# Optimization experiments

Hardware: AMD Instinct MI355X
Metric: run time of the kernel (lower is better)

## Reference

```python
import jax, jax.numpy as jnp
import numpy as np

EPS = 1e-12  # torch F.normalize clamp_min eps
NUM_HEADS = 4


def setup_inputs() -> dict:
    key = jax.random.key(0)
    ks = jax.random.split(key, 6)
    B, N, C = 8, 8192, 256
    x1 = jax.random.normal(ks[0], (B, N, C), dtype=jnp.float32)
    x2 = jax.random.normal(ks[1], (B, N, C), dtype=jnp.float32)
    s = 1.0 / np.sqrt(C)
    Wq = jax.random.normal(ks[2], (C, C), dtype=jnp.float32) * s
    Wk = jax.random.normal(ks[3], (C, C), dtype=jnp.float32) * s
    Wv = jax.random.normal(ks[4], (C, C), dtype=jnp.float32) * s
    Wo = jax.random.normal(ks[5], (C, C), dtype=jnp.float32) * s
    bo = jnp.zeros((C,), dtype=jnp.float32)
    temperature = jnp.ones((NUM_HEADS, 1, 1), dtype=jnp.float32)
    return {"x1": x1, "x2": x2, "Wq": Wq, "Wk": Wk, "Wv": Wv,
            "Wo": Wo, "bo": bo, "temperature": temperature}


def reference(x1, x2, Wq, Wk, Wv, Wo, bo, temperature):
    B, N, C = x1.shape
    H = NUM_HEADS
    d = C // H
    # Linear projections (torch Linear: y = x W^T), then [B,H,d,N] layout
    q = (x1 @ Wq.T).reshape(B, N, H, d).transpose(0, 2, 3, 1)  # [B,H,d,N]
    k = (x2 @ Wk.T).reshape(B, N, H, d).transpose(0, 2, 3, 1)  # [B,H,d,N]
    v = (x2 @ Wv.T).reshape(B, N, H, d).transpose(0, 2, 3, 1)  # [B,H,d,N]
    # L2-normalize along the token axis (dim=-1)
    qn = q / jnp.maximum(jnp.linalg.norm(q, axis=-1, keepdims=True), EPS)
    kn = k / jnp.maximum(jnp.linalg.norm(k, axis=-1, keepdims=True), EPS)
    # Channel-wise cross-covariance attention: [B,H,d,d]
    attn = jnp.einsum('bhdn,bhen->bhde', qn, kn) * temperature
    attn = jax.nn.softmax(attn, axis=-1)
    # (dropout is identity in eval mode)
    x_cross = jnp.einsum('bhde,bhen->bhdn', attn, v)  # [B,H,d,N]
    x_cross = x_cross.transpose(0, 3, 1, 2).reshape(B, N, C)  # [B,N,C]
    return x_cross @ Wo.T + bo
```

## Files before the change

kernel.cpp:

```cpp
#include <hip/hip_runtime.h>
#include <hip/hip_bf16.h>

#define BDIM 8
#define NTOK 8192
#define CDIM 256
#define HEADS 4
#define DHEAD 64
#define MROWS (BDIM * NTOK)

typedef unsigned short ushort_t;
typedef short bf16x8 __attribute__((ext_vector_type(8)));
typedef float f32x4 __attribute__((ext_vector_type(4)));
typedef unsigned short u16x8 __attribute__((ext_vector_type(8)));

#define GLOAD16(g, l) __builtin_amdgcn_global_load_lds( \
    (const __attribute__((address_space(1))) unsigned int*)(g), \
    (__attribute__((address_space(3))) unsigned int*)(l), 16, 0, 0)

__device__ inline ushort_t f2bf(float f) {
    __hip_bfloat16 h = __float2bfloat16(f);
    return *reinterpret_cast<ushort_t*>(&h);
}

__global__ __launch_bounds__(256) void zero_kernel(float* __restrict__ p, int n) {
    int i = blockIdx.x * 256 + threadIdx.x;
    if (i < n) p[i] = 0.0f;
}

__global__ __launch_bounds__(256) void cvt_bf16(
    const float* __restrict__ x1, const float* __restrict__ x2,
    const float* __restrict__ Wq, const float* __restrict__ Wk,
    const float* __restrict__ Wv,
    ushort_t* __restrict__ xb1, ushort_t* __restrict__ xb2,
    ushort_t* __restrict__ Wqb, ushort_t* __restrict__ Wkb,
    ushort_t* __restrict__ Wvb)
{
    const float* s; ushort_t* d; int n;
    switch (blockIdx.y) {
        case 0: s = x1; d = xb1; n = 16777216; break;
        case 1: s = x2; d = xb2; n = 16777216; break;
        case 2: s = Wq; d = Wqb; n = 65536; break;
        case 3: s = Wk; d = Wkb; n = 65536; break;
        default: s = Wv; d = Wvb; n = 65536; break;
    }
    int i = (blockIdx.x * 256 + threadIdx.x) * 8;
    if (i >= n) return;
    float4 a = *(const float4*)&s[i];
    float4 b = *(const float4*)&s[i + 4];
    u16x8 o;
    o[0] = f2bf(a.x); o[1] = f2bf(a.y); o[2] = f2bf(a.z); o[3] = f2bf(a.w);
    o[4] = f2bf(b.x); o[5] = f2bf(b.y); o[6] = f2bf(b.z); o[7] = f2bf(b.w);
    *(u16x8*)&d[i] = o;
}

__global__ __launch_bounds__(256) void proj_mfma(
    const ushort_t* __restrict__ xb1, const ushort_t* __restrict__ xb2,
    const ushort_t* __restrict__ Wqb, const ushort_t* __restrict__ Wkb,
    const ushort_t* __restrict__ Wvb,
    ushort_t* __restrict__ qp, ushort_t* __restrict__ kp, ushort_t* __restrict__ vp,
    float* __restrict__ ssq, float* __restrict__ ssk)
{
    const ushort_t* A; const ushort_t* W; ushort_t* outp; float* ss;
    if (blockIdx.z == 0)      { A = xb1; W = Wqb; outp = qp; ss = ssq; }
    else if (blockIdx.z == 1) { A = xb2; W = Wkb; outp = kp; ss = ssk; }
    else                      { A = xb2; W = Wvb; outp = vp; ss = nullptr; }

    __shared__ ushort_t Asl[8192];
    __shared__ ushort_t Bsl[8192];
    __shared__ float colss[128];

    const int t = threadIdx.x;
    const int lane = t & 63, w = t >> 6;
    const int l16 = lane & 15, quad = lane >> 4;
    const int m0 = blockIdx.x * 128;
    const int c0 = blockIdx.y * 128;
    const int wm = (w >> 1) * 64, wn = (w & 1) * 64;

    f32x4 acc[4][4] = {};

    for (int k0 = 0; k0 < CDIM; k0 += 64) {
        __syncthreads();
#pragma unroll
        for (int r = 0; r < 4; ++r) {
            int slot = r * 256 + t;
            int kg = slot >> 7, m = slot & 127;
            GLOAD16(A + (size_t)(m0 + m) * CDIM + k0 + kg * 8,
                    &Asl[(size_t)(r * 256 + w * 64) * 8]);
        }
#pragma unroll
        for (int r = 0; r < 4; ++r) {
            int slot = r * 256 + t;
            int kg = slot >> 7, c = slot & 127;
            GLOAD16(W + (size_t)(c0 + c) * CDIM + k0 + kg * 8,
                    &Bsl[(size_t)(r * 256 + w * 64) * 8]);
        }
        __syncthreads();
#pragma unroll
        for (int ks = 0; ks < 2; ++ks) {
            const int kg = ks * 4 + quad;
            bf16x8 aF[4], bF[4];
#pragma unroll
            for (int i = 0; i < 4; ++i)
                aF[i] = *(const bf16x8*)&Asl[(size_t)(kg * 128 + wm + i * 16 + l16) * 8];
#pragma unroll
            for (int j = 0; j < 4; ++j)
                bF[j] = *(const bf16x8*)&Bsl[(size_t)(kg * 128 + wn + j * 16 + l16) * 8];
#pragma unroll
            for (int i = 0; i < 4; ++i)
#pragma unroll
                for (int j = 0; j < 4; ++j)
                    acc[i][j] = __builtin_amdgcn_mfma_f32_16x16x32_bf16(aF[i], bF[j], acc[i][j], 0, 0, 0);
        }
    }

#pragma unroll
    for (int i = 0; i < 4; ++i) {
#pragma unroll
        for (int j = 0; j < 4; ++j) {
            int col = c0 + wn + j * 16 + l16;
#pragma unroll
            for (int reg = 0; reg < 4; ++reg) {
                int row = m0 + wm + i * 16 + quad * 4 + reg;
                outp[(size_t)row * CDIM + col] = f2bf(acc[i][j][reg]);
            }
        }
    }

    if (ss) {
        if (t < 128) colss[t] = 0.0f;
        __syncthreads();
#pragma unroll
        for (int j = 0; j < 4; ++j) {
            float s = 0.0f;
#pragma unroll
            for (int i = 0; i < 4; ++i)
#pragma unroll
                for (int reg = 0; reg < 4; ++reg)
                    s += acc[i][j][reg] * acc[i][j][reg];
            atomicAdd(&colss[wn + j * 16 + l16], s);
        }
        __syncthreads();
        if (t < 128) {
            int b = m0 >> 13;
            atomicAdd(&ss[b * CDIM + c0 + t], colss[t]);
        }
    }
}

__global__ __launch_bounds__(256) void gram_mfma(
    const ushort_t* __restrict__ qp, const ushort_t* __restrict__ kp,
    float* __restrict__ G)
{
    constexpr int NS = 144;
    __shared__ ushort_t qs[64 * NS];
    __shared__ ushort_t ks2[64 * NS];
    __shared__ float gsum[4096];

    const int t = threadIdx.x;
    const int lane = t & 63, w = t >> 6;
    const int l16 = lane & 15, quad = lane >> 4;
    const int slab = blockIdx.x, h = blockIdx.y, b = blockIdx.z;
    const size_t base = (size_t)b * NTOK * CDIM + h * DHEAD;

    for (int i = t; i < 4096; i += 256) gsum[i] = 0.0f;

    f32x4 acc[4][4] = {};

    for (int n0 = slab * 512; n0 < slab * 512 + 512; n0 += 128) {
        __syncthreads();
#pragma unroll
        for (int r = 0; r < 4; ++r) {
            int idx = r * 256 + t;
            int n = idx & 127, c8 = idx >> 7;
            size_t g = base + (size_t)(n0 + n) * CDIM + c8 * 8;
            ushort4 qa = *(const ushort4*)&qp[g];
            ushort4 qb = *(const ushort4*)&qp[g + 4];
            ushort4 ka = *(const ushort4*)&kp[g];
            ushort4 kb = *(const ushort4*)&kp[g + 4];
            int c = c8 * 8;
            qs[(c + 0) * NS + n] = qa.x; qs[(c + 1) * NS + n] = qa.y;
            qs[(c + 2) * NS + n] = qa.z; qs[(c + 3) * NS + n] = qa.w;
            qs[(c + 4) * NS + n] = qb.x; qs[(c + 5) * NS + n] = qb.y;
            qs[(c + 6) * NS + n] = qb.z; qs[(c + 7) * NS + n] = qb.w;
            ks2[(c + 0) * NS + n] = ka.x; ks2[(c + 1) * NS + n] = ka.y;
            ks2[(c + 2) * NS + n] = ka.z; ks2[(c + 3) * NS + n] = ka.w;
            ks2[(c + 4) * NS + n] = kb.x; ks2[(c + 5) * NS + n] = kb.y;
            ks2[(c + 6) * NS + n] = kb.z; ks2[(c + 7) * NS + n] = kb.w;
        }
        __syncthreads();
        bf16x8 aF[4], bF[4];
#pragma unroll
        for (int i = 0; i < 4; ++i)
            aF[i] = *(const bf16x8*)&qs[(i * 16 + l16) * NS + w * 32 + quad * 8];
#pragma unroll
        for (int j = 0; j < 4; ++j)
            bF[j] = *(const bf16x8*)&ks2[(j * 16 + l16) * NS + w * 32 + quad * 8];
#pragma unroll
        for (int i = 0; i < 4; ++i)
#pragma unroll
            for (int j = 0; j < 4; ++j)
                acc[i][j] = __builtin_amdgcn_mfma_f32_16x16x32_bf16(aF[i], bF[j], acc[i][j], 0, 0, 0);
    }

    __syncthreads();
#pragma unroll
    for (int i = 0; i < 4; ++i)
#pragma unroll
        for (int j = 0; j < 4; ++j)
#pragma unroll
            for (int reg = 0; reg < 4; ++reg)
                atomicAdd(&gsum[(i * 16 + quad * 4 + reg) * 64 + j * 16 + l16], acc[i][j][reg]);
    __syncthreads();

    float* Gp = G + (size_t)(b * HEADS + h) * 4096;
    for (int i = t; i < 4096; i += 256) atomicAdd(&Gp[i], gsum[i]);
}

__global__ __launch_bounds__(64) void attn_softmax(
    float* __restrict__ G, const float* __restrict__ ssq,
    const float* __restrict__ ssk, const float* __restrict__ temp)
{
    const int h = blockIdx.x, b = blockIdx.y;
    const int d = threadIdx.x;
    __shared__ float nk[64];

    float nq = fmaxf(sqrtf(ssq[b * CDIM + h * DHEAD + d]), 1e-12f);
    nk[d]    = fmaxf(sqrtf(ssk[b * CDIM + h * DHEAD + d]), 1e-12f);
    __syncthreads();

    float* row = G + (size_t)(b * HEADS + h) * DHEAD * DHEAD + d * DHEAD;
    const float tmp = temp[h];

    float vals[64];
    float mx = -1e30f;
#pragma unroll
    for (int e = 0; e < 64; ++e) {
        float v = row[e] / (nq * nk[e]) * tmp;
        vals[e] = v;
        mx = fmaxf(mx, v);
    }
    float s = 0.0f;
#pragma unroll
    for (int e = 0; e < 64; ++e) {
        float ev = __expf(vals[e] - mx);
        vals[e] = ev;
        s += ev;
    }
    float inv = 1.0f / s;
#pragma unroll
    for (int e = 0; e < 64; ++e) row[e] = vals[e] * inv;
}

__global__ __launch_bounds__(256) void weff_kernel(
    const float* __restrict__ Wo, const float* __restrict__ attn,
    ushort_t* __restrict__ Weffb)
{
    const int h = blockIdx.x, b = blockIdx.y;
    const int c = threadIdx.x;
    __shared__ float at[64][65];

    const float* Ab = attn + (size_t)(b * HEADS + h) * DHEAD * DHEAD;
    for (int idx = c; idx < DHEAD * DHEAD; idx += 256)
        at[idx >> 6][idx & 63] = Ab[idx];
    __syncthreads();

    float wo[64];
#pragma unroll
    for (int d2 = 0; d2 < 64; ++d2) wo[d2] = Wo[(size_t)c * CDIM + h * DHEAD + d2];

    ushort_t* Wb = Weffb + (size_t)b * CDIM * CDIM + (size_t)c * CDIM + h * DHEAD;
#pragma unroll 4
    for (int e = 0; e < 64; ++e) {
        float s = 0.0f;
#pragma unroll
        for (int d2 = 0; d2 < 64; ++d2) s += wo[d2] * at[d2][e];
        Wb[e] = f2bf(s);
    }
}

__global__ __launch_bounds__(256) void out_mfma(
    const ushort_t* __restrict__ vp, const ushort_t* __restrict__ Weffb,
    const float* __restrict__ bo, float* __restrict__ out)
{
    __shared__ ushort_t Asl[8192];
    __shared__ ushort_t Bsl[8192];

    const int t = threadIdx.x;
    const int lane = t & 63, w = t >> 6;
    const int l16 = lane & 15, quad = lane >> 4;
    const int m0 = blockIdx.x * 128;
    const int c0 = blockIdx.y * 128;
    const int wm = (w >> 1) * 64, wn = (w & 1) * 64;
    const ushort_t* Wb = Weffb + (size_t)(m0 >> 13) * CDIM * CDIM;

    f32x4 acc[4][4] = {};

    for (int k0 = 0; k0 < CDIM; k0 += 64) {
        __syncthreads();
#pragma unroll
        for (int r = 0; r < 4; ++r) {
            int slot = r * 256 + t;
            int kg = slot >> 7, m = slot & 127;
            GLOAD16(vp + (size_t)(m0 + m) * CDIM + k0 + kg * 8,
                    &Asl[(size_t)(r * 256 + w * 64) * 8]);
        }
#pragma unroll
        for (int r = 0; r < 4; ++r) {
            int slot = r * 256 + t;
            int kg = slot >> 7, c = slot & 127;
            GLOAD16(Wb + (size_t)(c0 + c) * CDIM + k0 + kg * 8,
                    &Bsl[(size_t)(r * 256 + w * 64) * 8]);
        }
        __syncthreads();
#pragma unroll
        for (int ks = 0; ks < 2; ++ks) {
            const int kg = ks * 4 + quad;
            bf16x8 aF[4], bF[4];
#pragma unroll
            for (int i = 0; i < 4; ++i)
                aF[i] = *(const bf16x8*)&Asl[(size_t)(kg * 128 + wm + i * 16 + l16) * 8];
#pragma unroll
            for (int j = 0; j < 4; ++j)
                bF[j] = *(const bf16x8*)&Bsl[(size_t)(kg * 128 + wn + j * 16 + l16) * 8];
#pragma unroll
            for (int i = 0; i < 4; ++i)
#pragma unroll
                for (int j = 0; j < 4; ++j)
                    acc[i][j] = __builtin_amdgcn_mfma_f32_16x16x32_bf16(aF[i], bF[j], acc[i][j], 0, 0, 0);
        }
    }

#pragma unroll
    for (int i = 0; i < 4; ++i) {
#pragma unroll
        for (int j = 0; j < 4; ++j) {
            int col = c0 + wn + j * 16 + l16;
            float bias = bo[col];
#pragma unroll
            for (int reg = 0; reg < 4; ++reg) {
                int row = m0 + wm + i * 16 + quad * 4 + reg;
                out[(size_t)row * CDIM + col] = acc[i][j][reg] + bias;
            }
        }
    }
}

extern "C" void kernel_launch(void* const* d_in, const int* in_sizes, int n_in,
                              void* d_out, int out_size, void* d_ws, size_t ws_size,
                              hipStream_t stream) {
    const float* x1   = (const float*)d_in[0];
    const float* x2   = (const float*)d_in[1];
    const float* Wq   = (const float*)d_in[2];
    const float* Wk   = (const float*)d_in[3];
    const float* Wv   = (const float*)d_in[4];
    const float* Wo   = (const float*)d_in[5];
    const float* bo   = (const float*)d_in[6];
    const float* temp = (const float*)d_in[7];
    float* out = (float*)d_out;

    char* ws = (char*)d_ws;
    const size_t SZP = (size_t)MROWS * CDIM * sizeof(ushort_t);
    ushort_t* qp   = (ushort_t*)(ws);
    ushort_t* kp   = (ushort_t*)(ws + SZP);
    ushort_t* vp   = (ushort_t*)(ws + 2 * SZP);
    ushort_t* xb1  = (ushort_t*)(ws + 3 * SZP);
    ushort_t* xb2  = (ushort_t*)(ws + 4 * SZP);
    ushort_t* Wqb  = (ushort_t*)(ws + 5 * SZP);
    ushort_t* Wkb  = (ushort_t*)(ws + 5 * SZP + 131072);
    ushort_t* Wvb  = (ushort_t*)(ws + 5 * SZP + 262144);
    float*    ssq  = (float*)(ws + 5 * SZP + 393216);
    float*    ssk  = (float*)(ws + 5 * SZP + 401408);
    float*    G    = (float*)(ws + 5 * SZP + 409600);
    ushort_t* Weffb= (ushort_t*)(ws + 5 * SZP + 933888);

    zero_kernel<<<dim3((135168 + 255) / 256), dim3(256), 0, stream>>>(ssq, 135168);

    cvt_bf16<<<dim3(8192, 5), dim3(256), 0, stream>>>(
        x1, x2, Wq, Wk, Wv, xb1, xb2, Wqb, Wkb, Wvb);

    proj_mfma<<<dim3(MROWS / 128, CDIM / 128, 3), dim3(256), 0, stream>>>(
        xb1, xb2, Wqb, Wkb, Wvb, qp, kp, vp, ssq, ssk);

    gram_mfma<<<dim3(16, HEADS, BDIM), dim3(256), 0, stream>>>(qp, kp, G);

    attn_softmax<<<dim3(HEADS, BDIM), dim3(64), 0, stream>>>(G, ssq, ssk, temp);

    weff_kernel<<<dim3(HEADS, BDIM), dim3(256), 0, stream>>>(Wo, G, Weffb);

    out_mfma<<<dim3(MROWS / 128, CDIM / 128), dim3(256), 0, stream>>>(vp, Weffb, bo, out);
}
```

Measured before the change: 367.8 us.

## Fuse bf16 conversion into projection GEMM and double-buffer LDS tiles

Removes the separate fp32-to-bf16 conversion kernel: the projection GEMM now reads fp32 inputs and weights directly, converts them in registers and writes bf16 into double-buffered LDS. Next-tile global loads are issued into registers before the barrier so they overlap the MFMA work. The output GEMM uses the same register-prefetch, double-buffered scheme, and the gram kernel stages its transpose with vector loads and 4-wide LDS stores. This drops a full write and re-read of the bf16 activation copies. In exchange each projection block re-reads fp32 inputs twice as wide, and it loses the async global-to-LDS loads and the 64-wide k-step.

```diff
diff --git a/kernel.cpp b/kernel.cpp
--- a/kernel.cpp
+++ b/kernel.cpp
@@ -12,105 +12,92 @@
 typedef short bf16x8 __attribute__((ext_vector_type(8)));
 typedef float f32x4 __attribute__((ext_vector_type(4)));
 typedef unsigned short u16x8 __attribute__((ext_vector_type(8)));
-
-#define GLOAD16(g, l) __builtin_amdgcn_global_load_lds( \
-    (const __attribute__((address_space(1))) unsigned int*)(g), \
-    (__attribute__((address_space(3))) unsigned int*)(l), 16, 0, 0)
+typedef unsigned short u16x4 __attribute__((ext_vector_type(4)));
 
 __device__ inline ushort_t f2bf(float f) {
     __hip_bfloat16 h = __float2bfloat16(f);
     return *reinterpret_cast<ushort_t*>(&h);
 }
 
+__device__ inline u16x8 pack8(float4 a, float4 b) {
+    u16x8 o;
+    o[0] = f2bf(a.x); o[1] = f2bf(a.y); o[2] = f2bf(a.z); o[3] = f2bf(a.w);
+    o[4] = f2bf(b.x); o[5] = f2bf(b.y); o[6] = f2bf(b.z); o[7] = f2bf(b.w);
+    return o;
+}
+
 __global__ __launch_bounds__(256) void zero_kernel(float* __restrict__ p, int n) {
     int i = blockIdx.x * 256 + threadIdx.x;
     if (i < n) p[i] = 0.0f;
 }
 
-__global__ __launch_bounds__(256) void cvt_bf16(
+__global__ __launch_bounds__(256) void proj_mfma(
     const float* __restrict__ x1, const float* __restrict__ x2,
     const float* __restrict__ Wq, const float* __restrict__ Wk,
     const float* __restrict__ Wv,
-    ushort_t* __restrict__ xb1, ushort_t* __restrict__ xb2,
-    ushort_t* __restrict__ Wqb, ushort_t* __restrict__ Wkb,
-    ushort_t* __restrict__ Wvb)
-{
-    const float* s; ushort_t* d; int n;
-    switch (blockIdx.y) {
-        case 0: s = x1; d = xb1; n = 16777216; break;
-        case 1: s = x2; d = xb2; n = 16777216; break;
-        case 2: s = Wq; d = Wqb; n = 65536; break;
-        case 3: s = Wk; d = Wkb; n = 65536; break;
-        default: s = Wv; d = Wvb; n = 65536; break;
-    }
-    int i = (blockIdx.x * 256 + threadIdx.x) * 8;
-    if (i >= n) return;
-    float4 a = *(const float4*)&s[i];
-    float4 b = *(const float4*)&s[i + 4];
-    u16x8 o;
-    o[0] = f2bf(a.x); o[1] = f2bf(a.y); o[2] = f2bf(a.z); o[3] = f2bf(a.w);
-    o[4] = f2bf(b.x); o[5] = f2bf(b.y); o[6] = f2bf(b.z); o[7] = f2bf(b.w);
-    *(u16x8*)&d[i] = o;
-}
-
-__global__ __launch_bounds__(256) void proj_mfma(
-    const ushort_t* __restrict__ xb1, const ushort_t* __restrict__ xb2,
-    const ushort_t* __restrict__ Wqb, const ushort_t* __restrict__ Wkb,
-    const ushort_t* __restrict__ Wvb,
     ushort_t* __restrict__ qp, ushort_t* __restrict__ kp, ushort_t* __restrict__ vp,
     float* __restrict__ ssq, float* __restrict__ ssk)
 {
-    const ushort_t* A; const ushort_t* W; ushort_t* outp; float* ss;
-    if (blockIdx.z == 0)      { A = xb1; W = Wqb; outp = qp; ss = ssq; }
-    else if (blockIdx.z == 1) { A = xb2; W = Wkb; outp = kp; ss = ssk; }
-    else                      { A = xb2; W = Wvb; outp = vp; ss = nullptr; }
-
-    __shared__ ushort_t Asl[8192];
-    __shared__ ushort_t Bsl[8192];
+    const float* A; const float* W; ushort_t* outp; float* ss;
+    if (blockIdx.z == 0)      { A = x1; W = Wq; outp = qp; ss = ssq; }
+    else if (blockIdx.z == 1) { A = x2; W = Wk; outp = kp; ss = ssk; }
+    else                      { A = x2; W = Wv; outp = vp; ss = nullptr; }
+
+    __shared__ ushort_t Asl[2][4096];
+    __shared__ ushort_t Bsl[2][4096];
     __shared__ float colss[128];
 
     const int t = threadIdx.x;
     const int lane = t & 63, w = t >> 6;
     const int l16 = lane & 15, quad = lane >> 4;
-    const int m0 = blockIdx.x * 128;
-    const int c0 = blockIdx.y * 128;
+    const int m0 = blockIdx.x * 128, c0 = blockIdx.y * 128;
     const int wm = (w >> 1) * 64, wn = (w & 1) * 64;
 
+    const int srow = t >> 1;
+    const int skh  = t & 1;
+
+    const float* Ap = A + (size_t)(m0 + srow) * CDIM + skh * 16;
+    const float* Wp = W + (size_t)(c0 + srow) * CDIM + skh * 16;
+
+    float4 ga[4], gb[4];
+#pragma unroll
+    for (int i = 0; i < 4; ++i) {
+        ga[i] = *(const float4*)(Ap + i * 4);
+        gb[i] = *(const float4*)(Wp + i * 4);
+    }
+
     f32x4 acc[4][4] = {};
 
-    for (int k0 = 0; k0 < CDIM; k0 += 64) {
-        __syncthreads();
-#pragma unroll
-        for (int r = 0; r < 4; ++r) {
-            int slot = r * 256 + t;
-            int kg = slot >> 7, m = slot & 127;
-            GLOAD16(A + (size_t)(m0 + m) * CDIM + k0 + kg * 8,
-                    &Asl[(size_t)(r * 256 + w * 64) * 8]);
-        }
-#pragma unroll
-        for (int r = 0; r < 4; ++r) {
-            int slot = r * 256 + t;
-            int kg = slot >> 7, c = slot & 127;
-            GLOAD16(W + (size_t)(c0 + c) * CDIM + k0 + kg * 8,
-                    &Bsl[(size_t)(r * 256 + w * 64) * 8]);
-        }
-        __syncthreads();
-#pragma unroll
-        for (int ks = 0; ks < 2; ++ks) {
-            const int kg = ks * 4 + quad;
-            bf16x8 aF[4], bF[4];
-#pragma unroll
-            for (int i = 0; i < 4; ++i)
-                aF[i] = *(const bf16x8*)&Asl[(size_t)(kg * 128 + wm + i * 16 + l16) * 8];
+#pragma unroll 2
+    for (int it = 0; it < 8; ++it) {
+        ushort_t* As = Asl[it & 1];
+        ushort_t* Bs = Bsl[it & 1];
+        *(u16x8*)&As[(skh * 2 + 0) * 1024 + srow * 8] = pack8(ga[0], ga[1]);
+        *(u16x8*)&As[(skh * 2 + 1) * 1024 + srow * 8] = pack8(ga[2], ga[3]);
+        *(u16x8*)&Bs[(skh * 2 + 0) * 1024 + srow * 8] = pack8(gb[0], gb[1]);
+        *(u16x8*)&Bs[(skh * 2 + 1) * 1024 + srow * 8] = pack8(gb[2], gb[3]);
+        if (it < 7) {
+            int ko = (it + 1) * 32;
+#pragma unroll
+            for (int i = 0; i < 4; ++i) {
+                ga[i] = *(const float4*)(Ap + ko + i * 4);
+                gb[i] = *(const float4*)(Wp + ko + i * 4);
+            }
+        }
+        asm volatile("s_waitcnt lgkmcnt(0)" ::: "memory");
+        __builtin_amdgcn_s_barrier();
+        bf16x8 aF[4], bF[4];
+#pragma unroll
+        for (int i = 0; i < 4; ++i)
+            aF[i] = *(const bf16x8*)&As[quad * 1024 + (wm + i * 16 + l16) * 8];
+#pragma unroll
+        for (int j = 0; j < 4; ++j)
+            bF[j] = *(const bf16x8*)&Bs[quad * 1024 + (wn + j * 16 + l16) * 8];
+#pragma unroll
+        for (int i = 0; i < 4; ++i)
 #pragma unroll
             for (int j = 0; j < 4; ++j)
-                bF[j] = *(const bf16x8*)&Bsl[(size_t)(kg * 128 + wn + j * 16 + l16) * 8];
-#pragma unroll
-            for (int i = 0; i < 4; ++i)
-#pragma unroll
-                for (int j = 0; j < 4; ++j)
-                    acc[i][j] = __builtin_amdgcn_mfma_f32_16x16x32_bf16(aF[i], bF[j], acc[i][j], 0, 0, 0);
-        }
+                acc[i][j] = __builtin_amdgcn_mfma_f32_16x16x32_bf16(aF[i], bF[j], acc[i][j], 0, 0, 0);
     }
 
 #pragma unroll
@@ -127,6 +114,7 @@
     }
 
     if (ss) {
+        __syncthreads();
         if (t < 128) colss[t] = 0.0f;
         __syncthreads();
 #pragma unroll
@@ -162,30 +150,29 @@
     const int slab = blockIdx.x, h = blockIdx.y, b = blockIdx.z;
     const size_t base = (size_t)b * NTOK * CDIM + h * DHEAD;
 
+    const int cg  = t >> 5;
+    const int ng4 = t & 31;
+
     for (int i = t; i < 4096; i += 256) gsum[i] = 0.0f;
 
     f32x4 acc[4][4] = {};
 
     for (int n0 = slab * 512; n0 < slab * 512 + 512; n0 += 128) {
-        __syncthreads();
-#pragma unroll
-        for (int r = 0; r < 4; ++r) {
-            int idx = r * 256 + t;
-            int n = idx & 127, c8 = idx >> 7;
-            size_t g = base + (size_t)(n0 + n) * CDIM + c8 * 8;
-            ushort4 qa = *(const ushort4*)&qp[g];
-            ushort4 qb = *(const ushort4*)&qp[g + 4];
-            ushort4 ka = *(const ushort4*)&kp[g];
-            ushort4 kb = *(const ushort4*)&kp[g + 4];
-            int c = c8 * 8;
-            qs[(c + 0) * NS + n] = qa.x; qs[(c + 1) * NS + n] = qa.y;
-            qs[(c + 2) * NS + n] = qa.z; qs[(c + 3) * NS + n] = qa.w;
-            qs[(c + 4) * NS + n] = qb.x; qs[(c + 5) * NS + n] = qb.y;
-            qs[(c + 6) * NS + n] = qb.z; qs[(c + 7) * NS + n] = qb.w;
-            ks2[(c + 0) * NS + n] = ka.x; ks2[(c + 1) * NS + n] = ka.y;
-            ks2[(c + 2) * NS + n] = ka.z; ks2[(c + 3) * NS + n] = ka.w;
-            ks2[(c + 4) * NS + n] = kb.x; ks2[(c + 5) * NS + n] = kb.y;
-            ks2[(c + 6) * NS + n] = kb.z; ks2[(c + 7) * NS + n] = kb.w;
+        u16x8 qv[4], kv[4];
+#pragma unroll
+        for (int i = 0; i < 4; ++i) {
+            size_t g = base + (size_t)(n0 + ng4 * 4 + i) * CDIM + cg * 8;
+            qv[i] = *(const u16x8*)&qp[g];
+            kv[i] = *(const u16x8*)&kp[g];
+        }
+        __syncthreads();
+#pragma unroll
+        for (int j = 0; j < 8; ++j) {
+            u16x4 wq, wk;
+            wq[0] = qv[0][j]; wq[1] = qv[1][j]; wq[2] = qv[2][j]; wq[3] = qv[3][j];
+            wk[0] = kv[0][j]; wk[1] = kv[1][j]; wk[2] = kv[2][j]; wk[3] = kv[3][j];
+            *(u16x4*)&qs[(cg * 8 + j) * NS + ng4 * 4] = wq;
+            *(u16x4*)&ks2[(cg * 8 + j) * NS + ng4 * 4] = wk;
         }
         __syncthreads();
         bf16x8 aF[4], bF[4];
@@ -282,52 +269,56 @@
     const ushort_t* __restrict__ vp, const ushort_t* __restrict__ Weffb,
     const float* __restrict__ bo, float* __restrict__ out)
 {
-    __shared__ ushort_t Asl[8192];
-    __shared__ ushort_t Bsl[8192];
+    __shared__ ushort_t Asl[2][4096];
+    __shared__ ushort_t Bsl[2][4096];
 
     const int t = threadIdx.x;
     const int lane = t & 63, w = t >> 6;
     const int l16 = lane & 15, quad = lane >> 4;
-    const int m0 = blockIdx.x * 128;
-    const int c0 = blockIdx.y * 128;
+    const int m0 = blockIdx.x * 128, c0 = blockIdx.y * 128;
     const int wm = (w >> 1) * 64, wn = (w & 1) * 64;
-    const ushort_t* Wb = Weffb + (size_t)(m0 >> 13) * CDIM * CDIM;
+
+    const int srow = t >> 1;
+    const int skh  = t & 1;
+
+    const ushort_t* Ap = vp + (size_t)(m0 + srow) * CDIM + skh * 16;
+    const ushort_t* Bp = Weffb + (size_t)(m0 >> 13) * CDIM * CDIM
+                       + (size_t)(c0 + srow) * CDIM + skh * 16;
+
+    u16x8 ga0 = *(const u16x8*)Ap,       ga1 = *(const u16x8*)(Ap + 8);
+    u16x8 gb0 = *(const u16x8*)Bp,       gb1 = *(const u16x8*)(Bp + 8);
 
     f32x4 acc[4][4] = {};
 
-    for (int k0 = 0; k0 < CDIM; k0 += 64) {
-        __syncthreads();
-#pragma unroll
-        for (int r = 0; r < 4; ++r) {
-            int slot = r * 256 + t;
-            int kg = slot >> 7, m = slot & 127;
-            GLOAD16(vp + (size_t)(m0 + m) * CDIM + k0 + kg * 8,
-                    &Asl[(size_t)(r * 256 + w * 64) * 8]);
-        }
-#pragma unroll
-        for (int r = 0; r < 4; ++r) {
-            int slot = r * 256 + t;
-            int kg = slot >> 7, c = slot & 127;
-            GLOAD16(Wb + (size_t)(c0 + c) * CDIM + k0 + kg * 8,
-                    &Bsl[(size_t)(r * 256 + w * 64) * 8]);
-        }
-        __syncthreads();
-#pragma unroll
-        for (int ks = 0; ks < 2; ++ks) {
-            const int kg = ks * 4 + quad;
-            bf16x8 aF[4], bF[4];
-#pragma unroll
-            for (int i = 0; i < 4; ++i)
-                aF[i] = *(const bf16x8*)&Asl[(size_t)(kg * 128 + wm + i * 16 + l16) * 8];
+#pragma unroll 2
+    for (int it = 0; it < 8; ++it) {
+        ushort_t* As = Asl[it & 1];
+        ushort_t* Bs = Bsl[it & 1];
+        *(u16x8*)&As[(skh * 2 + 0) * 1024 + srow * 8] = ga0;
+        *(u16x8*)&As[(skh * 2 + 1) * 1024 + srow * 8] = ga1;
+        *(u16x8*)&Bs[(skh * 2 + 0) * 1024 + srow * 8] = gb0;
+        *(u16x8*)&Bs[(skh * 2 + 1) * 1024 + srow * 8] = gb1;
+        if (it < 7) {
+            int ko = (it + 1) * 32;
+            ga0 = *(const u16x8*)(Ap + ko);
+            ga1 = *(const u16x8*)(Ap + ko + 8);
+            gb0 = *(const u16x8*)(Bp + ko);
+            gb1 = *(const u16x8*)(Bp + ko + 8);
+        }
+        asm volatile("s_waitcnt lgkmcnt(0)" ::: "memory");
+        __builtin_amdgcn_s_barrier();
+        bf16x8 aF[4], bF[4];
+#pragma unroll
+        for (int i = 0; i < 4; ++i)
+            aF[i] = *(const bf16x8*)&As[quad * 1024 + (wm + i * 16 + l16) * 8];
+#pragma unroll
+        for (int j = 0; j < 4; ++j)
+            bF[j] = *(const bf16x8*)&Bs[quad * 1024 + (wn + j * 16 + l16) * 8];
+#pragma unroll
+        for (int i = 0; i < 4; ++i)
 #pragma unroll
             for (int j = 0; j < 4; ++j)
-                bF[j] = *(const bf16x8*)&Bsl[(size_t)(kg * 128 + wn + j * 16 + l16) * 8];
-#pragma unroll
-            for (int i = 0; i < 4; ++i)
-#pragma unroll
-                for (int j = 0; j < 4; ++j)
-                    acc[i][j] = __builtin_amdgcn_mfma_f32_16x16x32_bf16(aF[i], bF[j], acc[i][j], 0, 0, 0);
-        }
+                acc[i][j] = __builtin_amdgcn_mfma_f32_16x16x32_bf16(aF[i], bF[j], acc[i][j], 0, 0, 0);
     }
 
 #pragma unroll
@@ -363,23 +354,15 @@
     ushort_t* qp   = (ushort_t*)(ws);
     ushort_t* kp   = (ushort_t*)(ws + SZP);
     ushort_t* vp   = (ushort_t*)(ws + 2 * SZP);
-    ushort_t* xb1  = (ushort_t*)(ws + 3 * SZP);
-    ushort_t* xb2  = (ushort_t*)(ws + 4 * SZP);
-    ushort_t* Wqb  = (ushort_t*)(ws + 5 * SZP);
-    ushort_t* Wkb  = (ushort_t*)(ws + 5 * SZP + 131072);
-    ushort_t* Wvb  = (ushort_t*)(ws + 5 * SZP + 262144);
-    float*    ssq  = (float*)(ws + 5 * SZP + 393216);
-    float*    ssk  = (float*)(ws + 5 * SZP + 401408);
-    float*    G    = (float*)(ws + 5 * SZP + 409600);
-    ushort_t* Weffb= (ushort_t*)(ws + 5 * SZP + 933888);
+    float*    ssq  = (float*)(ws + 3 * SZP);
+    float*    ssk  = (float*)(ws + 3 * SZP + 8192);
+    float*    G    = (float*)(ws + 3 * SZP + 16384);
+    ushort_t* Weffb= (ushort_t*)(ws + 3 * SZP + 540672);
 
     zero_kernel<<<dim3((135168 + 255) / 256), dim3(256), 0, stream>>>(ssq, 135168);
 
-    cvt_bf16<<<dim3(8192, 5), dim3(256), 0, stream>>>(
-        x1, x2, Wq, Wk, Wv, xb1, xb2, Wqb, Wkb, Wvb);
-
     proj_mfma<<<dim3(MROWS / 128, CDIM / 128, 3), dim3(256), 0, stream>>>(
-        xb1, xb2, Wqb, Wkb, Wvb, qp, kp, vp, ssq, ssk);
+        x1, x2, Wq, Wk, Wv, qp, kp, vp, ssq, ssk);
 
     gram_mfma<<<dim3(16, HEADS, BDIM), dim3(256), 0, stream>>>(qp, kp, G);
 
```

Measured after the change: 350.9 us. 4.6% less time.
